# Kernel optimization log

Hardware: AMD Instinct MI355X
Metric: run time of the kernel (lower is better)

The kernel has to match this reference:

```python
import jax, jax.numpy as jnp
import numpy as np

DIM = 1024
N_HEADS = 16
D_K = DIM // N_HEADS
B, N = 2, 2048


def _pairwise_dist(p):
    # p: [B, N, 3] -> Euclidean cdist [B, N, N], grad-safe at zero distance
    sq = jnp.sum(p * p, axis=-1)                      # [B, N]
    d2 = sq[:, :, None] + sq[:, None, :] - 2.0 * jnp.einsum('bnd,bmd->bnm', p, p)
    d2 = jnp.maximum(d2, 0.0)
    safe = jnp.where(d2 > 0.0, d2, 1.0)
    return jnp.where(d2 > 0.0, jnp.sqrt(safe), 0.0)


def setup_inputs() -> dict:
    key = jax.random.key(0)
    ks = jax.random.split(key, 11)
    s = 1.0 / np.sqrt(DIM)
    inp = {
        'x': jax.random.normal(ks[0], (B, N, DIM), jnp.float32),
        'positions': jax.random.normal(ks[1], (B, N, 3), jnp.float32),
        'W_q': jax.random.normal(ks[2], (DIM, DIM), jnp.float32) * s,
        'b_q': jnp.zeros((DIM,), jnp.float32),
        'W_k': jax.random.normal(ks[3], (DIM, DIM), jnp.float32) * s,
        'b_k': jnp.zeros((DIM,), jnp.float32),
        'W_v': jax.random.normal(ks[4], (DIM, DIM), jnp.float32) * s,
        'b_v': jnp.zeros((DIM,), jnp.float32),
        'W_o': jax.random.normal(ks[5], (DIM, DIM), jnp.float32) * s,
        'b_o': jnp.zeros((DIM,), jnp.float32),
        'dist_bias': jax.random.normal(ks[6], (N_HEADS, 1, 1), jnp.float32),
    }
    return inp


def reference(x, positions, W_q, b_q, W_k, b_k, W_v, b_v, W_o, b_o, dist_bias):
    Bv, Nv, C = x.shape
    def proj(W, b):
        # [B,N,C] -> [B,H,N,d_k]
        return (x @ W.T + b).reshape(Bv, Nv, N_HEADS, D_K).transpose(0, 2, 1, 3)
    Q = proj(W_q, b_q)
    K = proj(W_k, b_k)
    V = proj(W_v, b_v)
    attn = jnp.einsum('bhnd,bhmd->bhnm', Q, K) / np.sqrt(D_K)  # [B,H,N,N]
    dists = _pairwise_dist(positions)                          # [B,N,N]
    # log(exp(-|b|*d) + 1e-8), per-head bias broadcast over [B,H,N,N]
    dist_weights = jnp.exp(-jnp.abs(dist_bias)[None] * dists[:, None])
    attn = attn + jnp.log(dist_weights + 1e-8)
    attn = jax.nn.softmax(attn, axis=-1)
    out = jnp.einsum('bhnm,bhmd->bhnd', attn, V)               # [B,H,N,d_k]
    out = out.transpose(0, 2, 1, 3).reshape(Bv, Nv, C)
    return out @ W_o.T + b_o
```

## Files before the change

### kernel.cpp

```cpp
#include <hip/hip_runtime.h>
#include <hip/hip_bf16.h>
#include <stdint.h>

using bf16   = __hip_bfloat16;
using short8 = __attribute__((ext_vector_type(8))) short;
using f32x4  = __attribute__((ext_vector_type(4))) float;
using f32x16 = __attribute__((ext_vector_type(16))) float;

#define NSEQ   2048
#define NHEADS 16
#define DK     64
#define DMODEL 1024

#define GLDS16(gp, lp) __builtin_amdgcn_global_load_lds( \
    (const __attribute__((address_space(1))) void*)(gp), \
    (__attribute__((address_space(3))) void*)(lp), 16, 0, 0)

__device__ __forceinline__ ushort f2bf(float f){
  bf16 h = __float2bfloat16(f);
  return __builtin_bit_cast(ushort, h);
}
__device__ __forceinline__ float bf2f(ushort u){
  uint t = ((uint)u)<<16; return __builtin_bit_cast(float, t);
}

__global__ void k_cvt(const float4* __restrict__ src, ushort4* __restrict__ dst, int n4){
  int i = blockIdx.x*blockDim.x + threadIdx.x;
  if (i >= n4) return;
  float4 v = src[i];
  ushort4 o;
  o.x = f2bf(v.x); o.y = f2bf(v.y); o.z = f2bf(v.z); o.w = f2bf(v.w);
  dst[i] = o;
}

__global__ void k_geo(const float* __restrict__ pos, ushort* __restrict__ AF,
                      ushort* __restrict__ BF, int n){
  int i = blockIdx.x*blockDim.x + threadIdx.x;
  if (i >= n) return;
  float x = pos[i*3+0], y = pos[i*3+1], z = pos[i*3+2];
  float sq = x*x + y*y + z*z;
  ushort xh = f2bf(x);  float xhf = bf2f(xh);  ushort xl = f2bf(x - xhf);
  ushort yh = f2bf(y);  float yhf = bf2f(yh);  ushort yl = f2bf(y - yhf);
  ushort zh = f2bf(z);  float zhf = bf2f(zh);  ushort zl = f2bf(z - zhf);
  ushort sh = f2bf(sq); float shf = bf2f(sh);  ushort sl = f2bf(sq - shf);
  ushort m2xh = f2bf(-2.f*xhf), m2xl = f2bf(-2.f*bf2f(xl));
  ushort m2yh = f2bf(-2.f*yhf), m2yl = f2bf(-2.f*bf2f(yl));
  ushort m2zh = f2bf(-2.f*zhf), m2zl = f2bf(-2.f*bf2f(zl));
  const ushort one = 0x3F80;
  ushort af[16] = {xh,xl,xh, yh,yl,yh, zh,zl,zh, sh,sl, one,one, 0,0,0};
  ushort bv[16] = {m2xh,m2xh,m2xl, m2yh,m2yh,m2yl, m2zh,m2zh,m2zl, one,one, sh,sl, 0,0,0};
  *(uint4*)&AF[i*16]     = *(uint4*)&af[0];
  *(uint4*)&AF[i*16 + 8] = *(uint4*)&af[8];
  *(uint4*)&BF[i*16]     = *(uint4*)&bv[0];
  *(uint4*)&BF[i*16 + 8] = *(uint4*)&bv[8];
}

__device__ __forceinline__ void gemm_core(
    const ushort* __restrict__ Ap, const ushort* __restrict__ Bp,
    int bm, int bn, int tid, ushort smem[2][2][4096], f32x4 (&acc)[4][4])
{
  const int wave = tid>>6, lane = tid&63;
  const int wr = wave>>1, wc = wave&1;
  const int ko   = (lane>>4)*8;
  const int srow = wave*16 + (lane>>2);
  const int scol = (lane&3)*8;

  const ushort* As = Ap + (size_t)(bm*128)*DMODEL + scol;
  const ushort* Bs = Bp + (size_t)(bn*128)*DMODEL + scol;

#define STAGE(buf, kt) do { \
    _Pragma("unroll") \
    for (int i_=0;i_<2;i_++){ \
      GLDS16(As + (size_t)(i_*64 + srow)*DMODEL + (kt)*32, &smem[buf][0][i_*2048 + wave*512]); \
      GLDS16(Bs + (size_t)(i_*64 + srow)*DMODEL + (kt)*32, &smem[buf][1][i_*2048 + wave*512]); \
    } } while(0)

  STAGE(0, 0);
  for (int kt=0; kt<32; ++kt){
    int cur = kt&1;
    __syncthreads();
    if (kt<31) STAGE(cur^1, kt+1);
    short8 af[4], bfv[4];
    const ushort* At = smem[cur][0];
    const ushort* Bt = smem[cur][1];
    #pragma unroll
    for (int mi=0;mi<4;mi++) af[mi]  = *(const short8*)&At[(wr*64+mi*16+(lane&15))*32 + ko];
    #pragma unroll
    for (int ni=0;ni<4;ni++) bfv[ni] = *(const short8*)&Bt[(wc*64+ni*16+(lane&15))*32 + ko];
    #pragma unroll
    for (int mi=0;mi<4;mi++)
      #pragma unroll
      for (int ni=0;ni<4;ni++)
        acc[mi][ni] = __builtin_amdgcn_mfma_f32_16x16x32_bf16(af[mi], bfv[ni], acc[mi][ni], 0,0,0);
  }
#undef STAGE
}

__global__ __launch_bounds__(256) void k_gemm_qkv(
    const ushort* __restrict__ xb,
    const ushort* __restrict__ Wqb, const ushort* __restrict__ Wkb, const ushort* __restrict__ Wvb,
    const float* __restrict__ bq, const float* __restrict__ bk, const float* __restrict__ bv,
    ushort* __restrict__ Qo, ushort* __restrict__ Ko, ushort* __restrict__ Vto)
{
  __shared__ ushort smem[2][2][4096];
  const int tid = threadIdx.x;
  const int t = blockIdx.x & 255;
  const int z = blockIdx.x >> 8;
  const int lane = tid&63, wave = tid>>6;
  const int wr = wave>>1, wc = wave&1;

  const ushort* Ap; const ushort* Bp; const float* bias;
  ushort* outp; int bm, bn; float scale = 1.0f;
  if (z==0){ Ap=xb;  Bp=Wqb; bias=bq; outp=Qo;  bm=t>>3; bn=t&7; scale=0.125f; }
  else if (z==1){ Ap=xb;  Bp=Wkb; bias=bk; outp=Ko;  bm=t>>3; bn=t&7; }
  else          { Ap=Wvb; Bp=xb;  bias=bv; outp=Vto; bm=t&7;  bn=t>>3; }

  f32x4 acc[4][4] = {};
  gemm_core(Ap, Bp, bm, bn, tid, smem, acc);

  if (z<2){
    #pragma unroll
    for (int mi=0;mi<4;mi++){
      const int m0 = bm*128 + wr*64 + mi*16 + (lane>>4)*4;
      #pragma unroll
      for (int ni=0;ni<4;ni++){
        const int nn = bn*128 + wc*64 + ni*16 + (lane&15);
        const float bs = bias[nn];
        const int h = nn>>6, d = nn&63;
        #pragma unroll
        for (int j=0;j<4;j++){
          int mm = m0+j;
          int b = mm>>11, nr = mm&2047;
          size_t off = (((size_t)(b*NHEADS+h)*NSEQ) + nr)*DK + d;
          outp[off] = f2bf((acc[mi][ni][j] + bs)*scale);
        }
      }
    }
  } else {
    #pragma unroll
    for (int mi=0;mi<4;mi++){
      const int m0 = bm*128 + wr*64 + mi*16 + (lane>>4)*4;
      #pragma unroll
      for (int ni=0;ni<4;ni++){
        const int nn = bn*128 + wc*64 + ni*16 + (lane&15);
        const int b = nn>>11, nr = nn&2047;
        #pragma unroll
        for (int j=0;j<4;j++){
          int mm = m0+j;
          const float bs = bias[mm];
          int h = mm>>6, d = mm&63;
          size_t off = (((size_t)(b*NHEADS+h)*DK) + d)*NSEQ + nr;
          outp[off] = f2bf(acc[mi][ni][j] + bs);
        }
      }
    }
  }
}

__global__ __launch_bounds__(256) void k_gemm_out(
    const ushort* __restrict__ Ob, const ushort* __restrict__ Wob,
    const float* __restrict__ bo, float* __restrict__ out)
{
  __shared__ ushort smem[2][2][4096];
  const int tid = threadIdx.x;
  const int t = blockIdx.x;
  const int lane = tid&63, wave = tid>>6;
  const int wr = wave>>1, wc = wave&1;
  const int bm = t>>3, bn = t&7;
  f32x4 acc[4][4] = {};
  gemm_core(Ob, Wob, bm, bn, tid, smem, acc);
  #pragma unroll
  for (int mi=0;mi<4;mi++){
    const int m0 = bm*128 + wr*64 + mi*16 + (lane>>4)*4;
    #pragma unroll
    for (int ni=0;ni<4;ni++){
      const int nn = bn*128 + wc*64 + ni*16 + (lane&15);
      const float bs = bo[nn];
      #pragma unroll
      for (int j=0;j<4;j++)
        out[(size_t)(m0+j)*DMODEL + nn] = acc[mi][ni][j] + bs;
    }
  }
}

__global__ __launch_bounds__(256) void k_attn(
    const ushort* __restrict__ Q, const ushort* __restrict__ K, const ushort* __restrict__ Vt,
    const ushort* __restrict__ AF, const ushort* __restrict__ BF,
    const float* __restrict__ dist_bias,
    ushort* __restrict__ O)
{
  __shared__ float red[2][2048];
  __shared__ float lred[4][32];
  const int tid = threadIdx.x, wave = tid>>6, lane = tid&63;
  const int qt = blockIdx.x, h = blockIdx.y, b = blockIdx.z;
  const int lo5 = lane&31, hi = lane>>5;
  const float ah = fabsf(dist_bias[h]);
  const ushort* Qh  = Q  + ((size_t)(b*NHEADS+h))*NSEQ*DK;
  const ushort* Kh  = K  + ((size_t)(b*NHEADS+h))*NSEQ*DK;
  const ushort* Vth = Vt + ((size_t)(b*NHEADS+h))*DK*NSEQ;
  const ushort* AFb = AF + (size_t)b*NSEQ*16;
  const ushort* BFb = BF + (size_t)b*NSEQ*16;

  const int q0 = qt*32;

  short8 qf[4];
  #pragma unroll
  for (int s=0;s<4;s++)
    qf[s] = *(const short8*)&Qh[(size_t)(q0+lo5)*DK + s*16 + hi*8];
  const short8 bfq = *(const short8*)&BFb[(size_t)(q0+lo5)*16 + hi*8];

  f32x16 o0 = {}, o1 = {};
  float l_run = 0.f;
  const int j0 = wave*512;

  for (int jt=0; jt<16; ++jt){
    const int jb = j0 + jt*32;
    const short8 afk = *(const short8*)&AFb[(size_t)(jb+lo5)*16 + hi*8];
    f32x16 zz = {};
    f32x16 d2 = __builtin_amdgcn_mfma_f32_32x32x16_bf16(afk, bfq, zz, 0,0,0);
    f32x16 st = {};
    #pragma unroll
    for (int s=0;s<4;s++){
      short8 kf = *(const short8*)&Kh[(size_t)(jb+lo5)*DK + s*16 + hi*8];
      st = __builtin_amdgcn_mfma_f32_32x32x16_bf16(kf, qf[s], st, 0,0,0);
    }
    const short8 v00 = *(const short8*)&Vth[(size_t)(lo5)*NSEQ      + jb      + hi*8];
    const short8 v01 = *(const short8*)&Vth[(size_t)(lo5)*NSEQ      + jb + 16 + hi*8];
    const short8 v10 = *(const short8*)&Vth[(size_t)(32+lo5)*NSEQ   + jb      + hi*8];
    const short8 v11 = *(const short8*)&Vth[(size_t)(32+lo5)*NSEQ   + jb + 16 + hi*8];
    float p[16];
    #pragma unroll
    for (int r=0;r<16;r++){
      float d = __builtin_amdgcn_sqrtf(fmaxf(d2[r], 0.f));
      p[r] = __expf(fmaf(-ah, d, st[r]));
    }
    float s01=p[0]+p[1], s23=p[2]+p[3], s45=p[4]+p[5], s67=p[6]+p[7];
    float s89=p[8]+p[9], sab=p[10]+p[11], scd=p[12]+p[13], sef=p[14]+p[15];
    float rsum = ((s01+s23)+(s45+s67)) + ((s89+sab)+(scd+sef));
    rsum += __shfl_xor(rsum, 32);
    l_run += rsum;
    #pragma unroll
    for (int s=0;s<2;s++){
      uint w0, w1, w2, w3;
      asm("v_cvt_pk_bf16_f32 %0, %1, %2" : "=v"(w0) : "v"(p[8*s+0]), "v"(p[8*s+1]));
      asm("v_cvt_pk_bf16_f32 %0, %1, %2" : "=v"(w2) : "v"(p[8*s+4]), "v"(p[8*s+5]));
      asm("v_cvt_pk_bf16_f32 %0, %1, %2" : "=v"(w1) : "v"(p[8*s+2]), "v"(p[8*s+3]));
      asm("v_cvt_pk_bf16_f32 %0, %1, %2" : "=v"(w3) : "v"(p[8*s+6]), "v"(p[8*s+7]));
      asm volatile("v_permlane32_swap_b32 %0, %1" : "+v"(w0), "+v"(w2));
      asm volatile("v_permlane32_swap_b32 %0, %1" : "+v"(w1), "+v"(w3));
      uint4 aw; aw.x = w0; aw.y = w1; aw.z = w2; aw.w = w3;
      const short8 pa = __builtin_bit_cast(short8, aw);
      if (s==0){
        o0 = __builtin_amdgcn_mfma_f32_32x32x16_bf16(pa, v00, o0, 0,0,0);
        o1 = __builtin_amdgcn_mfma_f32_32x32x16_bf16(pa, v10, o1, 0,0,0);
      } else {
        o0 = __builtin_amdgcn_mfma_f32_32x32x16_bf16(pa, v01, o0, 0,0,0);
        o1 = __builtin_amdgcn_mfma_f32_32x32x16_bf16(pa, v11, o1, 0,0,0);
      }
    }
  }

#define STORE_ACC(buf) do { \
    float* rb = red[buf]; \
    _Pragma("unroll") \
    for (int g=0; g<8; ++g){ \
      const int sl = (g + lane) & 7; \
      float4 t; \
      if (g<4){ t.x=o0[g*4]; t.y=o0[g*4+1]; t.z=o0[g*4+2]; t.w=o0[g*4+3]; } \
      else    { t.x=o1[(g-4)*4]; t.y=o1[(g-4)*4+1]; t.z=o1[(g-4)*4+2]; t.w=o1[(g-4)*4+3]; } \
      *(float4*)&rb[lane*32 + sl*4] = t; \
    } } while(0)
#define LOAD_ADD_ACC(buf) do { \
    const float* rb = red[buf]; \
    _Pragma("unroll") \
    for (int g=0; g<8; ++g){ \
      const int sl = (g + lane) & 7; \
      float4 t = *(const float4*)&rb[lane*32 + sl*4]; \
      if (g<4){ o0[g*4]+=t.x; o0[g*4+1]+=t.y; o0[g*4+2]+=t.z; o0[g*4+3]+=t.w; } \
      else    { o1[(g-4)*4]+=t.x; o1[(g-4)*4+1]+=t.y; o1[(g-4)*4+2]+=t.z; o1[(g-4)*4+3]+=t.w; } \
    } } while(0)

  if (wave >= 2) STORE_ACC(wave-2);
  if (wave != 0 && hi == 0) lred[wave][lo5] = l_run;
  __syncthreads();
  if (wave < 2) LOAD_ADD_ACC(wave);
  __syncthreads();
  if (wave == 1) STORE_ACC(0);
  __syncthreads();
  if (wave == 0){
    LOAD_ADD_ACC(0);
    l_run += lred[1][lo5] + lred[2][lo5] + lred[3][lo5];
    #pragma unroll
    for (int r=0;r<16;r++){
      const int src = (r&3) + 8*(r>>2) + 4*hi;
      const float lr = __shfl(l_run, src);
      const float inv = 1.f/lr;
      const int i = q0 + src;
      O[((size_t)b*NSEQ + i)*DMODEL + h*DK + lo5]      = f2bf(o0[r]*inv);
      O[((size_t)b*NSEQ + i)*DMODEL + h*DK + 32 + lo5] = f2bf(o1[r]*inv);
    }
  }
#undef STORE_ACC
#undef LOAD_ADD_ACC
}

extern "C" void kernel_launch(void* const* d_in, const int* in_sizes, int n_in,
                              void* d_out, int out_size, void* d_ws, size_t ws_size,
                              hipStream_t stream) {
  const float* x   = (const float*)d_in[0];
  const float* pos = (const float*)d_in[1];
  const float* Wq  = (const float*)d_in[2];
  const float* bq  = (const float*)d_in[3];
  const float* Wk  = (const float*)d_in[4];
  const float* bk  = (const float*)d_in[5];
  const float* Wv  = (const float*)d_in[6];
  const float* bv  = (const float*)d_in[7];
  const float* Wo  = (const float*)d_in[8];
  const float* bo  = (const float*)d_in[9];
  const float* db  = (const float*)d_in[10];
  float* out = (float*)d_out;

  char* ws = (char*)d_ws;
  ushort* xb   = (ushort*)(ws);
  ushort* Wqb  = (ushort*)(ws + ((size_t)8<<20));
  ushort* Wkb  = (ushort*)(ws + ((size_t)10<<20));
  ushort* Wvb  = (ushort*)(ws + ((size_t)12<<20));
  ushort* Wob  = (ushort*)(ws + ((size_t)14<<20));
  ushort* Qb   = (ushort*)(ws + ((size_t)16<<20));
  ushort* Kb   = (ushort*)(ws + ((size_t)24<<20));
  ushort* Vtb  = (ushort*)(ws + ((size_t)32<<20));
  ushort* AFt  = Wqb;
  ushort* BFt  = (ushort*)(ws + ((size_t)8<<20) + (128<<10));
  ushort* Omrg = xb;

  k_cvt<<<4096, 256, 0, stream>>>((const float4*)x,  (ushort4*)xb,  1048576);
  k_cvt<<<1024, 256, 0, stream>>>((const float4*)Wq, (ushort4*)Wqb, 262144);
  k_cvt<<<1024, 256, 0, stream>>>((const float4*)Wk, (ushort4*)Wkb, 262144);
  k_cvt<<<1024, 256, 0, stream>>>((const float4*)Wv, (ushort4*)Wvb, 262144);
  k_cvt<<<1024, 256, 0, stream>>>((const float4*)Wo, (ushort4*)Wob, 262144);
  k_gemm_qkv<<<768, 256, 0, stream>>>(xb, Wqb, Wkb, Wvb, bq, bk, bv, Qb, Kb, Vtb);
  k_geo<<<16, 256, 0, stream>>>(pos, AFt, BFt, 2*NSEQ);
  k_attn<<<dim3(64,NHEADS,2), 256, 0, stream>>>(Qb, Kb, Vtb, AFt, BFt, db, Omrg);
  k_gemm_out<<<256, 256, 0, stream>>>(Omrg, Wob, bo, out);
}
```

Before: 294.2 us.

## Share K/V tiles in LDS across four query waves instead of splitting keys

The attention kernel is restructured so each block handles 128 queries, one 32-query slice per wave, and every wave walks all keys. K and V tiles are staged into double-buffered, XOR-swizzled LDS with async global-to-LDS loads, so the four waves share one copy of each tile instead of each wave reading K/V straight from global memory. This removes the cross-wave LDS reduction of partial outputs and row sums at the end. In exchange the grid shrinks to a quarter as many blocks, which lowers parallelism and occupancy, and a block barrier is added on every key tile.

```diff
diff --git a/kernel.cpp b/kernel.cpp
--- a/kernel.cpp
+++ b/kernel.cpp
@@ -68,18 +68,18 @@
   const ushort* As = Ap + (size_t)(bm*128)*DMODEL + scol;
   const ushort* Bs = Bp + (size_t)(bn*128)*DMODEL + scol;
 
-#define STAGE(buf, kt) do { \
+#define STAGEG(buf, kt) do { \
     _Pragma("unroll") \
     for (int i_=0;i_<2;i_++){ \
       GLDS16(As + (size_t)(i_*64 + srow)*DMODEL + (kt)*32, &smem[buf][0][i_*2048 + wave*512]); \
       GLDS16(Bs + (size_t)(i_*64 + srow)*DMODEL + (kt)*32, &smem[buf][1][i_*2048 + wave*512]); \
     } } while(0)
 
-  STAGE(0, 0);
+  STAGEG(0, 0);
   for (int kt=0; kt<32; ++kt){
     int cur = kt&1;
     __syncthreads();
-    if (kt<31) STAGE(cur^1, kt+1);
+    if (kt<31) STAGEG(cur^1, kt+1);
     short8 af[4], bfv[4];
     const ushort* At = smem[cur][0];
     const ushort* Bt = smem[cur][1];
@@ -93,7 +93,7 @@
       for (int ni=0;ni<4;ni++)
         acc[mi][ni] = __builtin_amdgcn_mfma_f32_16x16x32_bf16(af[mi], bfv[ni], acc[mi][ni], 0,0,0);
   }
-#undef STAGE
+#undef STAGEG
 }
 
 __global__ __launch_bounds__(256) void k_gemm_qkv(
@@ -189,8 +189,8 @@
     const float* __restrict__ dist_bias,
     ushort* __restrict__ O)
 {
-  __shared__ float red[2][2048];
-  __shared__ float lred[4][32];
+  __shared__ ushort kb[2][4096];
+  __shared__ ushort vb[2][4096];
   const int tid = threadIdx.x, wave = tid>>6, lane = tid&63;
   const int qt = blockIdx.x, h = blockIdx.y, b = blockIdx.z;
   const int lo5 = lane&31, hi = lane>>5;
@@ -201,7 +201,7 @@
   const ushort* AFb = AF + (size_t)b*NSEQ*16;
   const ushort* BFb = BF + (size_t)b*NSEQ*16;
 
-  const int q0 = qt*32;
+  const int q0 = qt*128 + wave*32;
 
   short8 qf[4];
   #pragma unroll
@@ -209,99 +209,87 @@
     qf[s] = *(const short8*)&Qh[(size_t)(q0+lo5)*DK + s*16 + hi*8];
   const short8 bfq = *(const short8*)&BFb[(size_t)(q0+lo5)*16 + hi*8];
 
+  const int grow  = lane>>3;
+  const int gc16  = (lane&7) ^ grow;
+  const int rowb  = wave*8 + grow;
+
+#define STAGE(buf, jb) do { \
+    _Pragma("unroll") \
+    for (int p_=0;p_<2;p_++){ \
+      const int rw_ = p_*32 + rowb; \
+      GLDS16(Kh  + (size_t)((jb)+rw_)*DK   + gc16*8, &kb[buf][(p_*256 + wave*64)*8]); \
+      GLDS16(Vth + (size_t)rw_*NSEQ + (jb) + gc16*8, &vb[buf][(p_*256 + wave*64)*8]); \
+    } } while(0)
+
+  const int rb = lo5*64;
+  const int rx = lo5 & 7;
+
   f32x16 o0 = {}, o1 = {};
   float l_run = 0.f;
-  const int j0 = wave*512;
-
-  for (int jt=0; jt<16; ++jt){
-    const int jb = j0 + jt*32;
-    const short8 afk = *(const short8*)&AFb[(size_t)(jb+lo5)*16 + hi*8];
-    f32x16 zz = {};
-    f32x16 d2 = __builtin_amdgcn_mfma_f32_32x32x16_bf16(afk, bfq, zz, 0,0,0);
-    f32x16 st = {};
-    #pragma unroll
-    for (int s=0;s<4;s++){
-      short8 kf = *(const short8*)&Kh[(size_t)(jb+lo5)*DK + s*16 + hi*8];
-      st = __builtin_amdgcn_mfma_f32_32x32x16_bf16(kf, qf[s], st, 0,0,0);
-    }
-    const short8 v00 = *(const short8*)&Vth[(size_t)(lo5)*NSEQ      + jb      + hi*8];
-    const short8 v01 = *(const short8*)&Vth[(size_t)(lo5)*NSEQ      + jb + 16 + hi*8];
-    const short8 v10 = *(const short8*)&Vth[(size_t)(32+lo5)*NSEQ   + jb      + hi*8];
-    const short8 v11 = *(const short8*)&Vth[(size_t)(32+lo5)*NSEQ   + jb + 16 + hi*8];
-    float p[16];
-    #pragma unroll
-    for (int r=0;r<16;r++){
-      float d = __builtin_amdgcn_sqrtf(fmaxf(d2[r], 0.f));
-      p[r] = __expf(fmaf(-ah, d, st[r]));
-    }
-    float s01=p[0]+p[1], s23=p[2]+p[3], s45=p[4]+p[5], s67=p[6]+p[7];
-    float s89=p[8]+p[9], sab=p[10]+p[11], scd=p[12]+p[13], sef=p[14]+p[15];
-    float rsum = ((s01+s23)+(s45+s67)) + ((s89+sab)+(scd+sef));
-    rsum += __shfl_xor(rsum, 32);
-    l_run += rsum;
-    #pragma unroll
-    for (int s=0;s<2;s++){
-      uint w0, w1, w2, w3;
-      asm("v_cvt_pk_bf16_f32 %0, %1, %2" : "=v"(w0) : "v"(p[8*s+0]), "v"(p[8*s+1]));
-      asm("v_cvt_pk_bf16_f32 %0, %1, %2" : "=v"(w2) : "v"(p[8*s+4]), "v"(p[8*s+5]));
-      asm("v_cvt_pk_bf16_f32 %0, %1, %2" : "=v"(w1) : "v"(p[8*s+2]), "v"(p[8*s+3]));
-      asm("v_cvt_pk_bf16_f32 %0, %1, %2" : "=v"(w3) : "v"(p[8*s+6]), "v"(p[8*s+7]));
-      asm volatile("v_permlane32_swap_b32 %0, %1" : "+v"(w0), "+v"(w2));
-      asm volatile("v_permlane32_swap_b32 %0, %1" : "+v"(w1), "+v"(w3));
-      uint4 aw; aw.x = w0; aw.y = w1; aw.z = w2; aw.w = w3;
-      const short8 pa = __builtin_bit_cast(short8, aw);
-      if (s==0){
-        o0 = __builtin_amdgcn_mfma_f32_32x32x16_bf16(pa, v00, o0, 0,0,0);
-        o1 = __builtin_amdgcn_mfma_f32_32x32x16_bf16(pa, v10, o1, 0,0,0);
-      } else {
-        o0 = __builtin_amdgcn_mfma_f32_32x32x16_bf16(pa, v01, o0, 0,0,0);
-        o1 = __builtin_amdgcn_mfma_f32_32x32x16_bf16(pa, v11, o1, 0,0,0);
+
+  STAGE(0, 0);
+  for (int t=0; t<32; ++t){
+    const int cur = t&1;
+    __syncthreads();
+    if (t<31) STAGE(cur^1, (t+1)*64);
+    const ushort* kbc = kb[cur];
+    const ushort* vbc = vb[cur];
+    #pragma unroll
+    for (int ss=0; ss<2; ++ss){
+      const int jb = t*64 + ss*32;
+      const short8 afk = *(const short8*)&AFb[(size_t)(jb+lo5)*16 + hi*8];
+      f32x16 zz = {};
+      f32x16 d2 = __builtin_amdgcn_mfma_f32_32x32x16_bf16(afk, bfq, zz, 0,0,0);
+      const short8 kf0 = *(const short8*)&kbc[ss*2048 + rb + (((0+hi)^rx)<<3)];
+      const short8 kf1 = *(const short8*)&kbc[ss*2048 + rb + (((2+hi)^rx)<<3)];
+      const short8 kf2 = *(const short8*)&kbc[ss*2048 + rb + (((4+hi)^rx)<<3)];
+      const short8 kf3 = *(const short8*)&kbc[ss*2048 + rb + (((6+hi)^rx)<<3)];
+      f32x16 st = {};
+      st = __builtin_amdgcn_mfma_f32_32x32x16_bf16(kf0, qf[0], st, 0,0,0);
+      st = __builtin_amdgcn_mfma_f32_32x32x16_bf16(kf1, qf[1], st, 0,0,0);
+      st = __builtin_amdgcn_mfma_f32_32x32x16_bf16(kf2, qf[2], st, 0,0,0);
+      st = __builtin_amdgcn_mfma_f32_32x32x16_bf16(kf3, qf[3], st, 0,0,0);
+      float p[16];
+      #pragma unroll
+      for (int r=0;r<16;r++){
+        float d = __builtin_amdgcn_sqrtf(fmaxf(d2[r], 0.f));
+        p[r] = __expf(fmaf(-ah, d, st[r]));
+      }
+      float s01=p[0]+p[1], s23=p[2]+p[3], s45=p[4]+p[5], s67=p[6]+p[7];
+      float s89=p[8]+p[9], sab=p[10]+p[11], scd=p[12]+p[13], sef=p[14]+p[15];
+      float rsum = ((s01+s23)+(s45+s67)) + ((s89+sab)+(scd+sef));
+      rsum += __shfl_xor(rsum, 32);
+      l_run += rsum;
+      #pragma unroll
+      for (int s=0;s<2;s++){
+        uint w0, w1, w2, w3;
+        asm("v_cvt_pk_bf16_f32 %0, %1, %2" : "=v"(w0) : "v"(p[8*s+0]), "v"(p[8*s+1]));
+        asm("v_cvt_pk_bf16_f32 %0, %1, %2" : "=v"(w2) : "v"(p[8*s+4]), "v"(p[8*s+5]));
+        asm("v_cvt_pk_bf16_f32 %0, %1, %2" : "=v"(w1) : "v"(p[8*s+2]), "v"(p[8*s+3]));
+        asm("v_cvt_pk_bf16_f32 %0, %1, %2" : "=v"(w3) : "v"(p[8*s+6]), "v"(p[8*s+7]));
+        asm volatile("v_permlane32_swap_b32 %0, %1" : "+v"(w0), "+v"(w2));
+        asm volatile("v_permlane32_swap_b32 %0, %1" : "+v"(w1), "+v"(w3));
+        uint4 aw; aw.x = w0; aw.y = w1; aw.z = w2; aw.w = w3;
+        const short8 pa = __builtin_bit_cast(short8, aw);
+        const int jcol = (ss<<2) + 2*s + hi;
+        const short8 v0 = *(const short8*)&vbc[       rb + ((jcol^rx)<<3)];
+        const short8 v1 = *(const short8*)&vbc[2048 + rb + ((jcol^rx)<<3)];
+        o0 = __builtin_amdgcn_mfma_f32_32x32x16_bf16(pa, v0, o0, 0,0,0);
+        o1 = __builtin_amdgcn_mfma_f32_32x32x16_bf16(pa, v1, o1, 0,0,0);
       }
     }
   }
-
-#define STORE_ACC(buf) do { \
-    float* rb = red[buf]; \
-    _Pragma("unroll") \
-    for (int g=0; g<8; ++g){ \
-      const int sl = (g + lane) & 7; \
-      float4 t; \
-      if (g<4){ t.x=o0[g*4]; t.y=o0[g*4+1]; t.z=o0[g*4+2]; t.w=o0[g*4+3]; } \
-      else    { t.x=o1[(g-4)*4]; t.y=o1[(g-4)*4+1]; t.z=o1[(g-4)*4+2]; t.w=o1[(g-4)*4+3]; } \
-      *(float4*)&rb[lane*32 + sl*4] = t; \
-    } } while(0)
-#define LOAD_ADD_ACC(buf) do { \
-    const float* rb = red[buf]; \
-    _Pragma("unroll") \
-    for (int g=0; g<8; ++g){ \
-      const int sl = (g + lane) & 7; \
-      float4 t = *(const float4*)&rb[lane*32 + sl*4]; \
-      if (g<4){ o0[g*4]+=t.x; o0[g*4+1]+=t.y; o0[g*4+2]+=t.z; o0[g*4+3]+=t.w; } \
-      else    { o1[(g-4)*4]+=t.x; o1[(g-4)*4+1]+=t.y; o1[(g-4)*4+2]+=t.z; o1[(g-4)*4+3]+=t.w; } \
-    } } while(0)
-
-  if (wave >= 2) STORE_ACC(wave-2);
-  if (wave != 0 && hi == 0) lred[wave][lo5] = l_run;
-  __syncthreads();
-  if (wave < 2) LOAD_ADD_ACC(wave);
-  __syncthreads();
-  if (wave == 1) STORE_ACC(0);
-  __syncthreads();
-  if (wave == 0){
-    LOAD_ADD_ACC(0);
-    l_run += lred[1][lo5] + lred[2][lo5] + lred[3][lo5];
-    #pragma unroll
-    for (int r=0;r<16;r++){
-      const int src = (r&3) + 8*(r>>2) + 4*hi;
-      const float lr = __shfl(l_run, src);
-      const float inv = 1.f/lr;
-      const int i = q0 + src;
-      O[((size_t)b*NSEQ + i)*DMODEL + h*DK + lo5]      = f2bf(o0[r]*inv);
-      O[((size_t)b*NSEQ + i)*DMODEL + h*DK + 32 + lo5] = f2bf(o1[r]*inv);
-    }
-  }
-#undef STORE_ACC
-#undef LOAD_ADD_ACC
+#undef STAGE
+
+  #pragma unroll
+  for (int r=0;r<16;r++){
+    const int src = (r&3) + 8*(r>>2) + 4*hi;
+    const float lr = __shfl(l_run, src);
+    const float inv = 1.f/lr;
+    const int i = q0 + src;
+    O[((size_t)b*NSEQ + i)*DMODEL + h*DK + lo5]      = f2bf(o0[r]*inv);
+    O[((size_t)b*NSEQ + i)*DMODEL + h*DK + 32 + lo5] = f2bf(o1[r]*inv);
+  }
 }
 
 extern "C" void kernel_launch(void* const* d_in, const int* in_sizes, int n_in,
@@ -340,6 +328,6 @@
   k_cvt<<<1024, 256, 0, stream>>>((const float4*)Wo, (ushort4*)Wob, 262144);
   k_gemm_qkv<<<768, 256, 0, stream>>>(xb, Wqb, Wkb, Wvb, bq, bk, bv, Qb, Kb, Vtb);
   k_geo<<<16, 256, 0, stream>>>(pos, AFt, BFt, 2*NSEQ);
-  k_attn<<<dim3(64,NHEADS,2), 256, 0, stream>>>(Qb, Kb, Vtb, AFt, BFt, db, Omrg);
+  k_attn<<<dim3(16,NHEADS,2), 256, 0, stream>>>(Qb, Kb, Vtb, AFt, BFt, db, Omrg);
   k_gemm_out<<<256, 256, 0, stream>>>(Omrg, Wob, bo, out);
 }
```

Measured after the change: 237.1 us. -19.4%, faster.
